# Optimization experiments

Measured on AMD Instinct MI355X. Metric: run time of the kernel, lower is better.

## Reference

```python
import jax, jax.numpy as jnp
import numpy as np

NEG_BIG = -9e15  # matches torch's -9000000000000000.0 mask value


def _l2norm(x, eps=1e-12):
    # F.normalize(x, p=2, dim=1)
    n = jnp.sqrt(jnp.sum(x * x, axis=1, keepdims=True))
    return x / jnp.maximum(n, eps)


def _fusion_attribute(emb, att_emb, adj):
    # cosine similarity [N, M]
    sim = _l2norm(emb) @ _l2norm(att_emb).T
    sim = sim * adj
    # masked softmax over dim=1: zeros -> -9e15
    logits = jnp.where(sim != 0, sim, jnp.full_like(sim, NEG_BIG))
    attention = jax.nn.softmax(logits, axis=1)
    return attention @ att_emb


def setup_inputs() -> dict:
    key = jax.random.key(0)
    k1, k2, k3, k4 = jax.random.split(key, 4)
    U, I, D = 10000, 8000, 64
    users_emb = 0.1 * jax.random.normal(k1, (U, D), dtype=jnp.float32)  # init.normal_(std=0.1)
    items_emb = 0.1 * jax.random.normal(k2, (I, D), dtype=jnp.float32)
    Out_UserAttNets = (jax.random.uniform(k3, (U, I)) < 0.05).astype(jnp.float32)
    Out_ItemAttNets = (jax.random.uniform(k4, (I, U)) < 0.05).astype(jnp.float32)
    return {
        "num_users": U,
        "num_items": I,
        "users_emb": users_emb,
        "items_emb": items_emb,
        "Out_UserAttNets": Out_UserAttNets,
        "Out_ItemAttNets": Out_ItemAttNets,
    }


def reference(num_users, num_items, users_emb, items_emb, Out_UserAttNets, Out_ItemAttNets):
    out_useratt_emb = _fusion_attribute(users_emb, items_emb, Out_UserAttNets)
    out_itematt_emb = _fusion_attribute(items_emb, users_emb, Out_ItemAttNets)
    return (users_emb, items_emb, out_useratt_emb, out_itematt_emb)
```

## Files before the change

kernel.cpp:

```cpp
#include <hip/hip_runtime.h>
#include <math.h>

typedef float f32x4 __attribute__((ext_vector_type(4)));

#define SEGCAP 512
#define NSEG   4

__global__ __launch_bounds__(256) void rinv_kernel(const float* __restrict__ emb,
                                                   float* __restrict__ rinv, int nrows) {
    int lane = threadIdx.x & 63;
    int row  = (blockIdx.x << 2) + (threadIdx.x >> 6);
    if (row >= nrows) return;
    float x = emb[(size_t)row * 64 + lane];
    float s = x * x;
#pragma unroll
    for (int off = 32; off; off >>= 1) s += __shfl_xor(s, off, 64);
    if (lane == 0) rinv[row] = 1.0f / fmaxf(sqrtf(s), 1e-12f);
}

__global__ __launch_bounds__(256) void att_row_kernel(
    const float* __restrict__ users, const float* __restrict__ items,
    const float* __restrict__ adjU,  const float* __restrict__ adjI,
    const float* __restrict__ rinvU, const float* __restrict__ rinvI,
    float* __restrict__ outU, float* __restrict__ outI, int U, int I)
{
    __shared__ float q_lds[64];
    __shared__ int   cols_sh[NSEG * SEGCAP];
    __shared__ int   wnnz_sh[NSEG];
    __shared__ float red[4][64];
    __shared__ float wsum_sh[4];

    const int tid  = threadIdx.x;
    const int lane = tid & 63;
    const int wid  = tid >> 6;

    const float* qemb; const float* kvemb; const float* adj;
    const float* rq;   const float* rk;    float* outp;
    int M, row;
    if ((int)blockIdx.x < U) {
        row = blockIdx.x;     qemb = users; kvemb = items; adj = adjU;
        rq = rinvU; rk = rinvI; outp = outU; M = I;
    } else {
        row = blockIdx.x - U; qemb = items; kvemb = users; adj = adjI;
        rq = rinvI; rk = rinvU; outp = outI; M = U;
    }
    const float* adjrow = adj + (size_t)row * M;

    if (tid < 64) q_lds[tid] = qemb[(size_t)row * 64 + tid] * rq[row];
    __syncthreads();

    int wcount = 0;
    const int M4 = M >> 2;
    const unsigned long long lt = (1ULL << lane) - 1ULL;
    for (int i4 = tid; i4 < M4; i4 += 256) {
        f32x4 a = __builtin_nontemporal_load((const f32x4*)adjrow + i4);
#pragma unroll
        for (int j = 0; j < 4; ++j) {
            bool pred = (a[j] != 0.0f);
            unsigned long long mask = __ballot(pred);
            if (pred) {
                int pos = wcount + __popcll(mask & lt);
                if (pos < SEGCAP) cols_sh[wid * SEGCAP + pos] = (i4 << 2) + j;
            }
            wcount += __popcll(mask);
        }
    }
    wcount = __shfl(wcount, 0, 64);
    if ((M & 3) && wid == 0) {
        int idx = (M4 << 2) + lane;
        bool pred = (idx < M) && (adjrow[idx] != 0.0f);
        unsigned long long mask = __ballot(pred);
        if (pred) {
            int pos = wcount + __popcll(mask & lt);
            if (pos < SEGCAP) cols_sh[pos] = idx;
        }
        wcount += __popcll(mask);
    }
    if (lane == 0) wnnz_sh[wid] = wcount;
    __syncthreads();

    const int sub = lane & 3;
    const int grp = lane >> 2;

    f32x4 q4[4];
#pragma unroll
    for (int j = 0; j < 4; ++j) q4[j] = ((const f32x4*)q_lds)[sub * 4 + j];

    f32x4 acc4[4];
#pragma unroll
    for (int j = 0; j < 4; ++j) acc4[j] = (f32x4){0.f, 0.f, 0.f, 0.f};
    float wsum = 0.f;

    int cnt = wnnz_sh[wid]; if (cnt > SEGCAP) cnt = SEGCAP;
    const int* cp = cols_sh + wid * SEGCAP;
    for (int i = grp; i < cnt; i += 16) {
        int col = cp[i];
        float rkc = rk[col];
        const f32x4* kr = (const f32x4*)(kvemb + (size_t)col * 64) + sub * 4;
        f32x4 r[4];
        float d = 0.f;
#pragma unroll
        for (int j = 0; j < 4; ++j) {
            r[j] = kr[j];
#pragma unroll
            for (int c = 0; c < 4; ++c) d = fmaf(q4[j][c], r[j][c], d);
        }
        d += __shfl_xor(d, 1, 64);
        d += __shfl_xor(d, 2, 64);
        float sim = d * rkc;
        float w = (sim != 0.0f) ? expf(sim - 1.0f) : 0.0f;
#pragma unroll
        for (int j = 0; j < 4; ++j)
#pragma unroll
            for (int c = 0; c < 4; ++c) acc4[j][c] = fmaf(w, r[j][c], acc4[j][c]);
        if (sub == 0) wsum += w;
    }

#pragma unroll
    for (int off = 4; off <= 32; off <<= 1) {
        wsum += __shfl_xor(wsum, off, 64);
#pragma unroll
        for (int j = 0; j < 4; ++j) {
            f32x4 o;
#pragma unroll
            for (int c = 0; c < 4; ++c) o[c] = __shfl_xor(acc4[j][c], off, 64);
            acc4[j] += o;
        }
    }
    if (lane < 4) {
#pragma unroll
        for (int j = 0; j < 4; ++j)
            ((f32x4*)&red[wid][lane * 16])[j] = acc4[j];
    }
    if (lane == 0) wsum_sh[wid] = wsum;
    __syncthreads();

    if (wid == 0) {
        float tot = red[0][lane] + red[1][lane] + red[2][lane] + red[3][lane];
        float den = wsum_sh[0] + wsum_sh[1] + wsum_sh[2] + wsum_sh[3];
        float o;
        if (den > 0.0f) {
            o = tot / den;
        } else {
            float m = 0.f;
            for (int r = 0; r < M; ++r) m += kvemb[(size_t)r * 64 + lane];
            o = m / (float)M;
        }
        outp[(size_t)row * 64 + lane] = o;
    }
}

extern "C" void kernel_launch(void* const* d_in, const int* in_sizes, int n_in,
                              void* d_out, int out_size, void* d_ws, size_t ws_size,
                              hipStream_t stream) {
    const float* users = (const float*)d_in[2];
    const float* items = (const float*)d_in[3];
    const float* adjU  = (const float*)d_in[4];
    const float* adjI  = (const float*)d_in[5];
    const int U = in_sizes[2] / 64;
    const int I = in_sizes[3] / 64;

    float* out   = (float*)d_out;
    float* rinvU = (float*)d_ws;
    float* rinvI = rinvU + U;

    hipMemcpyAsync(out, users, (size_t)U * 64 * sizeof(float),
                   hipMemcpyDeviceToDevice, stream);
    hipMemcpyAsync(out + (size_t)U * 64, items, (size_t)I * 64 * sizeof(float),
                   hipMemcpyDeviceToDevice, stream);

    rinv_kernel<<<(U + 3) / 4, 256, 0, stream>>>(users, rinvU, U);
    rinv_kernel<<<(I + 3) / 4, 256, 0, stream>>>(items, rinvI, I);

    float* outUatt = out + (size_t)(U + I) * 64;
    float* outIatt = outUatt + (size_t)U * 64;
    att_row_kernel<<<U + I, 256, 0, stream>>>(users, items, adjU, adjI,
                                              rinvU, rinvI, outUatt, outIatt, U, I);
}
```

Measured before the change: 242.9 us.

## Map one wavefront per attention row and drop block-level syncs

```diff
diff --git a/kernel.cpp b/kernel.cpp
--- a/kernel.cpp
+++ b/kernel.cpp
@@ -3,19 +3,27 @@
 
 typedef float f32x4 __attribute__((ext_vector_type(4)));
 
-#define SEGCAP 512
-#define NSEG   4
+#define SEGCAP 768
 
-__global__ __launch_bounds__(256) void rinv_kernel(const float* __restrict__ emb,
-                                                   float* __restrict__ rinv, int nrows) {
+__global__ __launch_bounds__(256) void rinv_kernel(const float* __restrict__ users,
+                                                   const float* __restrict__ items,
+                                                   float* __restrict__ rinvU,
+                                                   float* __restrict__ rinvI,
+                                                   int U, int I) {
     int lane = threadIdx.x & 63;
     int row  = (blockIdx.x << 2) + (threadIdx.x >> 6);
-    if (row >= nrows) return;
-    float x = emb[(size_t)row * 64 + lane];
+    const float* src; float* dst;
+    if (row < U) {
+        src = users + (size_t)row * 64; dst = rinvU + row;
+    } else {
+        int r = row - U; if (r >= I) return;
+        src = items + (size_t)r * 64; dst = rinvI + r;
+    }
+    float x = src[lane];
     float s = x * x;
 #pragma unroll
     for (int off = 32; off; off >>= 1) s += __shfl_xor(s, off, 64);
-    if (lane == 0) rinv[row] = 1.0f / fmaxf(sqrtf(s), 1e-12f);
+    if (lane == 0) *dst = 1.0f / fmaxf(sqrtf(s), 1e-12f);
 }
 
 __global__ __launch_bounds__(256) void att_row_kernel(
@@ -24,35 +32,30 @@
     const float* __restrict__ rinvU, const float* __restrict__ rinvI,
     float* __restrict__ outU, float* __restrict__ outI, int U, int I)
 {
-    __shared__ float q_lds[64];
-    __shared__ int   cols_sh[NSEG * SEGCAP];
-    __shared__ int   wnnz_sh[NSEG];
-    __shared__ float red[4][64];
-    __shared__ float wsum_sh[4];
+    __shared__ int cols_sh[4][SEGCAP];
 
     const int tid  = threadIdx.x;
     const int lane = tid & 63;
     const int wid  = tid >> 6;
+    const int grow = (blockIdx.x << 2) + wid;
+    if (grow >= U + I) return;
 
     const float* qemb; const float* kvemb; const float* adj;
     const float* rq;   const float* rk;    float* outp;
     int M, row;
-    if ((int)blockIdx.x < U) {
-        row = blockIdx.x;     qemb = users; kvemb = items; adj = adjU;
+    if (grow < U) {
+        row = grow;     qemb = users; kvemb = items; adj = adjU;
         rq = rinvU; rk = rinvI; outp = outU; M = I;
     } else {
-        row = blockIdx.x - U; qemb = items; kvemb = users; adj = adjI;
+        row = grow - U; qemb = items; kvemb = users; adj = adjI;
         rq = rinvI; rk = rinvU; outp = outI; M = U;
     }
     const float* adjrow = adj + (size_t)row * M;
 
-    if (tid < 64) q_lds[tid] = qemb[(size_t)row * 64 + tid] * rq[row];
-    __syncthreads();
-
     int wcount = 0;
     const int M4 = M >> 2;
     const unsigned long long lt = (1ULL << lane) - 1ULL;
-    for (int i4 = tid; i4 < M4; i4 += 256) {
+    for (int i4 = lane; i4 < M4; i4 += 64) {
         f32x4 a = __builtin_nontemporal_load((const f32x4*)adjrow + i4);
 #pragma unroll
         for (int j = 0; j < 4; ++j) {
@@ -60,41 +63,42 @@
             unsigned long long mask = __ballot(pred);
             if (pred) {
                 int pos = wcount + __popcll(mask & lt);
-                if (pos < SEGCAP) cols_sh[wid * SEGCAP + pos] = (i4 << 2) + j;
+                if (pos < SEGCAP) cols_sh[wid][pos] = (i4 << 2) + j;
             }
             wcount += __popcll(mask);
         }
     }
     wcount = __shfl(wcount, 0, 64);
-    if ((M & 3) && wid == 0) {
+    if (M & 3) {
         int idx = (M4 << 2) + lane;
         bool pred = (idx < M) && (adjrow[idx] != 0.0f);
         unsigned long long mask = __ballot(pred);
         if (pred) {
             int pos = wcount + __popcll(mask & lt);
-            if (pos < SEGCAP) cols_sh[pos] = idx;
+            if (pos < SEGCAP) cols_sh[wid][pos] = idx;
         }
         wcount += __popcll(mask);
     }
-    if (lane == 0) wnnz_sh[wid] = wcount;
-    __syncthreads();
+    int cnt = wcount > SEGCAP ? SEGCAP : wcount;
 
     const int sub = lane & 3;
     const int grp = lane >> 2;
 
+    const float rqv = rq[row];
     f32x4 q4[4];
 #pragma unroll
-    for (int j = 0; j < 4; ++j) q4[j] = ((const f32x4*)q_lds)[sub * 4 + j];
+    for (int j = 0; j < 4; ++j)
+        q4[j] = ((const f32x4*)(qemb + (size_t)row * 64))[sub * 4 + j] * rqv;
 
     f32x4 acc4[4];
 #pragma unroll
     for (int j = 0; j < 4; ++j) acc4[j] = (f32x4){0.f, 0.f, 0.f, 0.f};
     float wsum = 0.f;
 
-    int cnt = wnnz_sh[wid]; if (cnt > SEGCAP) cnt = SEGCAP;
-    const int* cp = cols_sh + wid * SEGCAP;
+    const int* cp = cols_sh[wid];
+    int col = (grp < cnt) ? cp[grp] : 0;
     for (int i = grp; i < cnt; i += 16) {
-        int col = cp[i];
+        int ncol = (i + 16 < cnt) ? cp[i + 16] : 0;
         float rkc = rk[col];
         const f32x4* kr = (const f32x4*)(kvemb + (size_t)col * 64) + sub * 4;
         f32x4 r[4];
@@ -114,6 +118,7 @@
 #pragma unroll
             for (int c = 0; c < 4; ++c) acc4[j][c] = fmaf(w, r[j][c], acc4[j][c]);
         if (sub == 0) wsum += w;
+        col = ncol;
     }
 
 #pragma unroll
@@ -127,26 +132,28 @@
             acc4[j] += o;
         }
     }
+    float den = __shfl(wsum, 0, 64);
+
     if (lane < 4) {
+        float* orow = outp + (size_t)row * 64 + lane * 16;
+        if (den > 0.0f) {
+            float inv = 1.0f / den;
 #pragma unroll
-        for (int j = 0; j < 4; ++j)
-            ((f32x4*)&red[wid][lane * 16])[j] = acc4[j];
-    }
-    if (lane == 0) wsum_sh[wid] = wsum;
-    __syncthreads();
-
-    if (wid == 0) {
-        float tot = red[0][lane] + red[1][lane] + red[2][lane] + red[3][lane];
-        float den = wsum_sh[0] + wsum_sh[1] + wsum_sh[2] + wsum_sh[3];
-        float o;
-        if (den > 0.0f) {
-            o = tot / den;
+            for (int j = 0; j < 4; ++j)
+                ((f32x4*)orow)[j] = acc4[j] * inv;
         } else {
-            float m = 0.f;
-            for (int r = 0; r < M; ++r) m += kvemb[(size_t)r * 64 + lane];
-            o = m / (float)M;
+            f32x4 m[4];
+#pragma unroll
+            for (int j = 0; j < 4; ++j) m[j] = (f32x4){0.f, 0.f, 0.f, 0.f};
+            for (int r = 0; r < M; ++r) {
+                const f32x4* kr = (const f32x4*)(kvemb + (size_t)r * 64) + lane * 4;
+#pragma unroll
+                for (int j = 0; j < 4; ++j) m[j] += kr[j];
+            }
+            float invM = 1.0f / (float)M;
+#pragma unroll
+            for (int j = 0; j < 4; ++j) ((f32x4*)orow)[j] = m[j] * invM;
         }
-        outp[(size_t)row * 64 + lane] = o;
     }
 }
 
@@ -169,11 +176,10 @@
     hipMemcpyAsync(out + (size_t)U * 64, items, (size_t)I * 64 * sizeof(float),
                    hipMemcpyDeviceToDevice, stream);
 
-    rinv_kernel<<<(U + 3) / 4, 256, 0, stream>>>(users, rinvU, U);
-    rinv_kernel<<<(I + 3) / 4, 256, 0, stream>>>(items, rinvI, I);
+    rinv_kernel<<<(U + I + 3) / 4, 256, 0, stream>>>(users, items, rinvU, rinvI, U, I);
 
     float* outUatt = out + (size_t)(U + I) * 64;
     float* outIatt = outUatt + (size_t)U * 64;
-    att_row_kernel<<<U + I, 256, 0, stream>>>(users, items, adjU, adjI,
-                                              rinvU, rinvI, outUatt, outIatt, U, I);
+    att_row_kernel<<<(U + I + 3) / 4, 256, 0, stream>>>(users, items, adjU, adjI,
+                                                        rinvU, rinvI, outUatt, outIatt, U, I);
 }
```

Measured after the change: 248.1 us. +2.1%, slower.

## Replace sparse gather attention with dense bf16 MFMA flash-style split-K attention

Applied to the files above, without the earlier changes.

```diff
diff --git a/kernel.cpp b/kernel.cpp
--- a/kernel.cpp
+++ b/kernel.cpp
@@ -2,151 +2,198 @@
 #include <math.h>
 
 typedef float f32x4 __attribute__((ext_vector_type(4)));
-
-#define SEGCAP 512
-#define NSEG   4
-
-__global__ __launch_bounds__(256) void rinv_kernel(const float* __restrict__ emb,
-                                                   float* __restrict__ rinv, int nrows) {
+typedef short bf16x8 __attribute__((ext_vector_type(8)));
+typedef unsigned int u32;
+typedef unsigned short u16;
+
+#define SPLITS 2
+
+__device__ __forceinline__ u16 f2b(float x) {
+    union { float f; u32 u; } v; v.f = x;
+    return (u16)((v.u + 0x7FFFu + ((v.u >> 16) & 1u)) >> 16);
+}
+
+__global__ __launch_bounds__(256) void prep_kernel(
+    const float* __restrict__ users, const float* __restrict__ items,
+    u16* __restrict__ uhat, u16* __restrict__ ihat,
+    u16* __restrict__ uT,   u16* __restrict__ iT,
+    int U, int I, int Upad, int Ipad)
+{
     int lane = threadIdx.x & 63;
     int row  = (blockIdx.x << 2) + (threadIdx.x >> 6);
-    if (row >= nrows) return;
-    float x = emb[(size_t)row * 64 + lane];
+    const float* src; u16 *hat, *Tt; int N, Npad, r;
+    if (row < Upad) { r = row; src = users; hat = uhat; Tt = uT; N = U; Npad = Upad; }
+    else { r = row - Upad; if (r >= Ipad) return;
+           src = items; hat = ihat; Tt = iT; N = I; Npad = Ipad; }
+    float x = (r < N) ? src[(size_t)r * 64 + lane] : 0.0f;
     float s = x * x;
 #pragma unroll
     for (int off = 32; off; off >>= 1) s += __shfl_xor(s, off, 64);
-    if (lane == 0) rinv[row] = 1.0f / fmaxf(sqrtf(s), 1e-12f);
-}
-
-__global__ __launch_bounds__(256) void att_row_kernel(
+    float rinv = 1.0f / fmaxf(sqrtf(s), 1e-12f);
+    hat[(size_t)r * 64 + lane] = f2b(x * rinv);
+    Tt[(size_t)lane * Npad + r] = f2b(x);
+}
+
+__global__ __launch_bounds__(256, 2) void attn_kernel(
+    const u16* __restrict__ uhat, const u16* __restrict__ ihat,
+    const u16* __restrict__ uT,   const u16* __restrict__ iT,
+    const float* __restrict__ adjU, const float* __restrict__ adjI,
+    float* __restrict__ wsO, float* __restrict__ wsDen,
+    int U, int I, int Upad, int Ipad, int nbU, int nbI)
+{
+    __shared__ u16 Plds[4][16][72];
+
+    const int lane = threadIdx.x & 63;
+    const int wid  = threadIdx.x >> 6;
+    const int r15  = lane & 15;
+    const int g    = lane >> 4;
+    const int T    = U + I;
+
+    const int nbT = nbU + nbI;
+    const int s   = blockIdx.x / nbT;
+    const int b   = blockIdx.x % nbT;
+    const int dir = (b >= nbU);
+
+    int N, M, Mpad, rowoff, qg;
+    const u16 *qh, *kh, *vt;
+    const float* adj;
+    if (!dir) { N=U; M=I; Mpad=Ipad; qh=uhat; kh=ihat; vt=iT; adj=adjU; rowoff=0; qg = b*4 + wid; }
+    else      { N=I; M=U; Mpad=Upad; qh=ihat; kh=uhat; vt=uT; adj=adjI; rowoff=U; qg = (b-nbU)*4 + wid; }
+    const int qbase = qg << 4;
+    if (qbase >= N) return;
+
+    const int ntiles = (M + 63) >> 6;
+    const int t0 = (s * ntiles) / SPLITS, t1 = ((s + 1) * ntiles) / SPLITS;
+
+    const u16* qrowp = qh + (size_t)(qbase + r15) * 64 + g * 8;
+    bf16x8 qf0 = *(const bf16x8*)(qrowp);
+    bf16x8 qf1 = *(const bf16x8*)(qrowp + 32);
+
+    const f32x4 zero4 = (f32x4){0.f, 0.f, 0.f, 0.f};
+    f32x4 oacc[4];
+#pragma unroll
+    for (int d = 0; d < 4; ++d) oacc[d] = zero4;
+    float wsum = 0.f;
+
+    const float* adjrow = adj + (size_t)(qbase + r15) * M;
+
+    f32x4 adjc[4];
+    {
+        int tb = t0 << 6;
+#pragma unroll
+        for (int c = 0; c < 4; ++c) {
+            int cb = tb + c * 16;
+            adjc[c] = (cb < M) ? __builtin_nontemporal_load((const f32x4*)(adjrow + cb + g*4))
+                               : zero4;
+        }
+    }
+
+    for (int t = t0; t < t1; ++t) {
+        const int tb = t << 6;
+        bf16x8 kf[4][2];
+        bool cv[4];
+#pragma unroll
+        for (int c = 0; c < 4; ++c) {
+            int cb = tb + c * 16;
+            cv[c] = (cb < M);
+            if (cv[c]) {
+                const u16* kp = kh + (size_t)(cb + r15) * 64 + g * 8;
+                kf[c][0] = *(const bf16x8*)(kp);
+                kf[c][1] = *(const bf16x8*)(kp + 32);
+            }
+        }
+        bf16x8 vf[4][2];
+#pragma unroll
+        for (int d = 0; d < 4; ++d) {
+            const u16* vp = vt + (size_t)(d * 16 + r15) * Mpad + tb + g * 8;
+            vf[d][0] = *(const bf16x8*)(vp);
+            vf[d][1] = *(const bf16x8*)(vp + 32);
+        }
+        f32x4 adjn[4];
+        {
+            int tn = (t + 1 < t1) ? t + 1 : t;
+            int tb2 = tn << 6;
+#pragma unroll
+            for (int c = 0; c < 4; ++c) {
+                int cb = tb2 + c * 16;
+                adjn[c] = (cb < M) ? __builtin_nontemporal_load((const f32x4*)(adjrow + cb + g*4))
+                                   : zero4;
+            }
+        }
+
+        u32* prow = (u32*)(&Plds[wid][r15][0]);
+#pragma unroll
+        for (int c = 0; c < 4; ++c) {
+            u32 lo = 0, hi = 0;
+            if (cv[c]) {
+                f32x4 sa = __builtin_amdgcn_mfma_f32_16x16x32_bf16(kf[c][0], qf0, zero4, 0, 0, 0);
+                sa = __builtin_amdgcn_mfma_f32_16x16x32_bf16(kf[c][1], qf1, sa, 0, 0, 0);
+                float w0, w1, w2, w3;
+#pragma unroll
+                for (int j = 0; j < 4; ++j) {
+                    float sv = sa[j], av = adjc[c][j];
+                    float e  = __expf(sv - 1.0f);
+                    float wj = (av != 0.0f && sv != 0.0f) ? e : 0.0f;
+                    wsum += wj;
+                    if (j == 0) w0 = wj; else if (j == 1) w1 = wj;
+                    else if (j == 2) w2 = wj; else w3 = wj;
+                }
+                lo = (u32)f2b(w0) | ((u32)f2b(w1) << 16);
+                hi = (u32)f2b(w2) | ((u32)f2b(w3) << 16);
+            }
+            prow[c * 8 + g * 2]     = lo;
+            prow[c * 8 + g * 2 + 1] = hi;
+        }
+
+        bf16x8 pf0 = *(const bf16x8*)(&Plds[wid][r15][g * 8]);
+        bf16x8 pf1 = *(const bf16x8*)(&Plds[wid][r15][32 + g * 8]);
+#pragma unroll
+        for (int d = 0; d < 4; ++d) {
+            oacc[d] = __builtin_amdgcn_mfma_f32_16x16x32_bf16(vf[d][0], pf0, oacc[d], 0, 0, 0);
+            oacc[d] = __builtin_amdgcn_mfma_f32_16x16x32_bf16(vf[d][1], pf1, oacc[d], 0, 0, 0);
+        }
+#pragma unroll
+        for (int c = 0; c < 4; ++c) adjc[c] = adjn[c];
+    }
+
+    wsum += __shfl_xor(wsum, 16, 64);
+    wsum += __shfl_xor(wsum, 32, 64);
+
+    if (lane < 16)
+        wsDen[(size_t)s * T + rowoff + qbase + lane] = wsum;
+
+    float* obase = wsO + ((size_t)s * T + rowoff + qbase + r15) * 64;
+#pragma unroll
+    for (int d = 0; d < 4; ++d)
+#pragma unroll
+        for (int j = 0; j < 4; ++j)
+            obase[d * 16 + g * 4 + j] = oacc[d][j];
+}
+
+__global__ __launch_bounds__(256) void combine_kernel(
+    const float* __restrict__ wsO, const float* __restrict__ wsDen,
     const float* __restrict__ users, const float* __restrict__ items,
-    const float* __restrict__ adjU,  const float* __restrict__ adjI,
-    const float* __restrict__ rinvU, const float* __restrict__ rinvI,
     float* __restrict__ outU, float* __restrict__ outI, int U, int I)
 {
-    __shared__ float q_lds[64];
-    __shared__ int   cols_sh[NSEG * SEGCAP];
-    __shared__ int   wnnz_sh[NSEG];
-    __shared__ float red[4][64];
-    __shared__ float wsum_sh[4];
-
-    const int tid  = threadIdx.x;
-    const int lane = tid & 63;
-    const int wid  = tid >> 6;
-
-    const float* qemb; const float* kvemb; const float* adj;
-    const float* rq;   const float* rk;    float* outp;
-    int M, row;
-    if ((int)blockIdx.x < U) {
-        row = blockIdx.x;     qemb = users; kvemb = items; adj = adjU;
-        rq = rinvU; rk = rinvI; outp = outU; M = I;
+    int lane = threadIdx.x & 63;
+    int row  = (blockIdx.x << 2) + (threadIdx.x >> 6);
+    int T = U + I;
+    if (row >= T) return;
+    float den = 0.f, o = 0.f;
+#pragma unroll
+    for (int s = 0; s < SPLITS; ++s) {
+        den += wsDen[(size_t)s * T + row];
+        o   += wsO[((size_t)s * T + row) * 64 + lane];
+    }
+    float* outp = (row < U) ? (outU + (size_t)row * 64) : (outI + (size_t)(row - U) * 64);
+    if (den > 0.f) {
+        outp[lane] = o / den;
     } else {
-        row = blockIdx.x - U; qemb = items; kvemb = users; adj = adjI;
-        rq = rinvI; rk = rinvU; outp = outI; M = U;
-    }
-    const float* adjrow = adj + (size_t)row * M;
-
-    if (tid < 64) q_lds[tid] = qemb[(size_t)row * 64 + tid] * rq[row];
-    __syncthreads();
-
-    int wcount = 0;
-    const int M4 = M >> 2;
-    const unsigned long long lt = (1ULL << lane) - 1ULL;
-    for (int i4 = tid; i4 < M4; i4 += 256) {
-        f32x4 a = __builtin_nontemporal_load((const f32x4*)adjrow + i4);
-#pragma unroll
-        for (int j = 0; j < 4; ++j) {
-            bool pred = (a[j] != 0.0f);
-            unsigned long long mask = __ballot(pred);
-            if (pred) {
-                int pos = wcount + __popcll(mask & lt);
-                if (pos < SEGCAP) cols_sh[wid * SEGCAP + pos] = (i4 << 2) + j;
-            }
-            wcount += __popcll(mask);
-        }
-    }
-    wcount = __shfl(wcount, 0, 64);
-    if ((M & 3) && wid == 0) {
-        int idx = (M4 << 2) + lane;
-        bool pred = (idx < M) && (adjrow[idx] != 0.0f);
-        unsigned long long mask = __ballot(pred);
-        if (pred) {
-            int pos = wcount + __popcll(mask & lt);
-            if (pos < SEGCAP) cols_sh[pos] = idx;
-        }
-        wcount += __popcll(mask);
-    }
-    if (lane == 0) wnnz_sh[wid] = wcount;
-    __syncthreads();
-
-    const int sub = lane & 3;
-    const int grp = lane >> 2;
-
-    f32x4 q4[4];
-#pragma unroll
-    for (int j = 0; j < 4; ++j) q4[j] = ((const f32x4*)q_lds)[sub * 4 + j];
-
-    f32x4 acc4[4];
-#pragma unroll
-    for (int j = 0; j < 4; ++j) acc4[j] = (f32x4){0.f, 0.f, 0.f, 0.f};
-    float wsum = 0.f;
-
-    int cnt = wnnz_sh[wid]; if (cnt > SEGCAP) cnt = SEGCAP;
-    const int* cp = cols_sh + wid * SEGCAP;
-    for (int i = grp; i < cnt; i += 16) {
-        int col = cp[i];
-        float rkc = rk[col];
-        const f32x4* kr = (const f32x4*)(kvemb + (size_t)col * 64) + sub * 4;
-        f32x4 r[4];
-        float d = 0.f;
-#pragma unroll
-        for (int j = 0; j < 4; ++j) {
-            r[j] = kr[j];
-#pragma unroll
-            for (int c = 0; c < 4; ++c) d = fmaf(q4[j][c], r[j][c], d);
-        }
-        d += __shfl_xor(d, 1, 64);
-        d += __shfl_xor(d, 2, 64);
-        float sim = d * rkc;
-        float w = (sim != 0.0f) ? expf(sim - 1.0f) : 0.0f;
-#pragma unroll
-        for (int j = 0; j < 4; ++j)
-#pragma unroll
-            for (int c = 0; c < 4; ++c) acc4[j][c] = fmaf(w, r[j][c], acc4[j][c]);
-        if (sub == 0) wsum += w;
-    }
-
-#pragma unroll
-    for (int off = 4; off <= 32; off <<= 1) {
-        wsum += __shfl_xor(wsum, off, 64);
-#pragma unroll
-        for (int j = 0; j < 4; ++j) {
-            f32x4 o;
-#pragma unroll
-            for (int c = 0; c < 4; ++c) o[c] = __shfl_xor(acc4[j][c], off, 64);
-            acc4[j] += o;
-        }
-    }
-    if (lane < 4) {
-#pragma unroll
-        for (int j = 0; j < 4; ++j)
-            ((f32x4*)&red[wid][lane * 16])[j] = acc4[j];
-    }
-    if (lane == 0) wsum_sh[wid] = wsum;
-    __syncthreads();
-
-    if (wid == 0) {
-        float tot = red[0][lane] + red[1][lane] + red[2][lane] + red[3][lane];
-        float den = wsum_sh[0] + wsum_sh[1] + wsum_sh[2] + wsum_sh[3];
-        float o;
-        if (den > 0.0f) {
-            o = tot / den;
-        } else {
-            float m = 0.f;
-            for (int r = 0; r < M; ++r) m += kvemb[(size_t)r * 64 + lane];
-            o = m / (float)M;
-        }
-        outp[(size_t)row * 64 + lane] = o;
+        const float* kv = (row < U) ? items : users;
+        int M = (row < U) ? I : U;
+        float m = 0.f;
+        for (int r = 0; r < M; ++r) m += kv[(size_t)r * 64 + lane];
+        outp[lane] = m / (float)M;
     }
 }
 
@@ -159,21 +206,36 @@
     const float* adjI  = (const float*)d_in[5];
     const int U = in_sizes[2] / 64;
     const int I = in_sizes[3] / 64;
-
-    float* out   = (float*)d_out;
-    float* rinvU = (float*)d_ws;
-    float* rinvI = rinvU + U;
+    const int Upad = (U + 63) & ~63;
+    const int Ipad = (I + 63) & ~63;
+    const int T = U + I;
+
+    char* w = (char*)d_ws;
+    u16* uhat = (u16*)w;  w += (size_t)Upad * 64 * 2;
+    u16* ihat = (u16*)w;  w += (size_t)Ipad * 64 * 2;
+    u16* uT   = (u16*)w;  w += (size_t)Upad * 64 * 2;
+    u16* iT   = (u16*)w;  w += (size_t)Ipad * 64 * 2;
+    float* wsO   = (float*)w;  w += (size_t)SPLITS * T * 64 * sizeof(float);
+    float* wsDen = (float*)w;
+
+    float* out  = (float*)d_out;
+    float* outU = out + (size_t)T * 64;
+    float* outI = outU + (size_t)U * 64;
 
     hipMemcpyAsync(out, users, (size_t)U * 64 * sizeof(float),
                    hipMemcpyDeviceToDevice, stream);
     hipMemcpyAsync(out + (size_t)U * 64, items, (size_t)I * 64 * sizeof(float),
                    hipMemcpyDeviceToDevice, stream);
 
-    rinv_kernel<<<(U + 3) / 4, 256, 0, stream>>>(users, rinvU, U);
-    rinv_kernel<<<(I + 3) / 4, 256, 0, stream>>>(items, rinvI, I);
-
-    float* outUatt = out + (size_t)(U + I) * 64;
-    float* outIatt = outUatt + (size_t)U * 64;
-    att_row_kernel<<<U + I, 256, 0, stream>>>(users, items, adjU, adjI,
-                                              rinvU, rinvI, outUatt, outIatt, U, I);
-}
+    int prows = Upad + Ipad;
+    prep_kernel<<<(prows + 3) / 4, 256, 0, stream>>>(users, items, uhat, ihat,
+                                                     uT, iT, U, I, Upad, Ipad);
+
+    int nbU = ((U + 15) / 16 + 3) / 4;
+    int nbI = ((I + 15) / 16 + 3) / 4;
+    attn_kernel<<<SPLITS * (nbU + nbI), 256, 0, stream>>>(
+        uhat, ihat, uT, iT, adjU, adjI, wsO, wsDen, U, I, Upad, Ipad, nbU, nbI);
+
+    combine_kernel<<<(T + 3) / 4, 256, 0, stream>>>(wsO, wsDen, users, items,
+                                                    outU, outI, U, I);
+}
```

Measured after the change: 497.7 us. 2.05x slower.
